# Kernel tuning notes

Measured on AMD Instinct MI355X. Metric: run time of the kernel, lower is better.

Reference implementation:

```python
import jax, jax.numpy as jnp
import numpy as np

LEAKY_SLOPE = 0.2
N_HEADS = 8
INPUT_DIM = 128
HEAD_DIM = 16  # embed_dim=128 // n_heads=8


def setup_inputs() -> dict:
    key = jax.random.key(0)
    k1, k2, k3, k4 = jax.random.split(key, 4)
    b, n = 4, 512
    h = jax.random.normal(k1, (b, n, INPUT_DIM), dtype=jnp.float32)
    mask = jnp.zeros((b, n, n), dtype=bool)  # 1 = attention not possible
    stdv_w = 1.0 / np.sqrt(HEAD_DIM)
    Wl = jax.random.uniform(k2, (N_HEADS, INPUT_DIM, HEAD_DIM), minval=-stdv_w, maxval=stdv_w, dtype=jnp.float32)
    Wr = jax.random.uniform(k3, (N_HEADS, INPUT_DIM, HEAD_DIM), minval=-stdv_w, maxval=stdv_w, dtype=jnp.float32)
    # Wak in torch is (n_heads, head_dim, 1); stdv = 1/sqrt(size(-1)) = 1
    Wak = jax.random.uniform(k4, (N_HEADS, HEAD_DIM), minval=-1.0, maxval=1.0, dtype=jnp.float32)
    return {"h": h, "mask": mask, "Wl": Wl, "Wr": Wr, "Wak": Wak}


def reference(h, mask, Wl, Wr, Wak):
    b, n, _ = h.shape
    # per-head projections: g = h @ W  -> (heads, batch, N, head_dim)
    g_l = jnp.einsum('bni,hid->hbnd', h, Wl)
    g_r = jnp.einsum('bni,hid->hbnd', h, Wr)
    # additive attention: LeakyReLU(g_l_i + g_r_j) . a  -> (heads, batch, N, N)
    e = jax.nn.leaky_relu(g_l[:, :, :, None, :] + g_r[:, :, None, :, :],
                          negative_slope=LEAKY_SLOPE)
    scores = jnp.einsum('hbijd,hd->hbij', e, Wak)
    scores = jnp.where(mask[None], -jnp.inf, scores)
    attn = jax.nn.softmax(scores, axis=-1)
    # weighted sum of g_r, then ReLU; output layout (batch, N, heads*head_dim)
    h_prime = jax.nn.relu(jnp.einsum('hbij,hbjd->bihd', attn, g_r))
    return h_prime.reshape(b, n, -1)
```

## Files before the change

### kernel.cpp

```cpp
#include <hip/hip_runtime.h>
#include <hip/hip_bf16.h>

#define B_SZ 4
#define N_SZ 512
#define IN_DIM 128
#define NH 8
#define HD 16
#define SLOPE 0.2f

#define ROWS 32
#define JT   16
#define TPB  512
#define GR_STRIDE 18
#define HROW (IN_DIM + 1)

typedef float v2f __attribute__((ext_vector_type(2)));


__global__ __launch_bounds__(256) void proj_kernel(
    const float* __restrict__ hin, const float* __restrict__ Wl,
    const float* __restrict__ Wr, float* __restrict__ gl, float* __restrict__ gr)
{
    int row = blockIdx.x;
    __shared__ float hrow[IN_DIM];
    int t = threadIdx.x;
    if (t < IN_DIM) hrow[t] = hin[(size_t)row * IN_DIM + t];
    __syncthreads();

    int side = t >> 7;
    int hd = t & 127;
    int head = hd >> 4, d = hd & 15;
    const float* W = (side ? Wr : Wl) + head * (IN_DIM * HD) + d;
    float acc = 0.f;
#pragma unroll 16
    for (int k = 0; k < IN_DIM; ++k)
        acc = fmaf(hrow[k], W[k * HD], acc);

    int b = row >> 9, i = row & (N_SZ - 1);
    float* g = side ? gr : gl;
    g[((size_t)(head * B_SZ + b) * N_SZ + i) * HD + d] = acc;
}

__global__ __launch_bounds__(TPB, 4) void attn_kernel(
    const float* __restrict__ gl, const float* __restrict__ gr,
    const float* __restrict__ Wak, const unsigned char* __restrict__ mask,
    float* __restrict__ out)
{
    __shared__ float grs[N_SZ * GR_STRIDE];
    __shared__ float gls[ROWS * HD];
    __shared__ float crs[N_SZ];

    int bid = blockIdx.x;
    int itile = bid & 15;
    int hb = bid >> 4;
    int head = hb >> 2, b = hb & 3;
    int t = threadIdx.x;

    const float* grp = gr + (size_t)hb * (N_SZ * HD);
    for (int idx4 = t; idx4 < N_SZ * HD / 4; idx4 += TPB) {
        float4 v = ((const float4*)grp)[idx4];
        int j = idx4 >> 2, dq = (idx4 & 3) * 4;
        float* p = &grs[j * GR_STRIDE + dq];
        *(v2f*)p = (v2f){v.x, v.y};
        *(v2f*)(p + 2) = (v2f){v.z, v.w};
    }
    const float* glp = gl + ((size_t)hb * N_SZ + itile * ROWS) * HD;
    gls[t] = glp[t];
    __syncthreads();

    const float* ap = Wak + head * HD;

    {
        const float* r = &grs[t * GR_STRIDE];
        float acc = 0.f;
#pragma unroll
        for (int dd = 0; dd < HD; ++dd) acc = fmaf(ap[dd], r[dd], acc);
        crs[t] = 0.6f * acc;
    }
    __syncthreads();

    int il = t >> 4;
    int jt = t & 15;
    int i = itile * ROWS + il;

    v2f glv[HD / 2], o[HD / 2];
    float av04[HD];
    const float* grow = &gls[il * HD];
#pragma unroll
    for (int e = 0; e < HD / 2; ++e) glv[e] = *(const v2f*)(grow + 2 * e);
    float cl06;
    {
        float acc = 0.f;
#pragma unroll
        for (int dd = 0; dd < HD; ++dd) acc = fmaf(ap[dd], grow[dd], acc);
        cl06 = 0.6f * acc;
    }
#pragma unroll
    for (int dd = 0; dd < HD; ++dd) av04[dd] = 0.4f * ap[dd];
#pragma unroll
    for (int e = 0; e < HD / 2; ++e) o[e] = (v2f){0.f, 0.f};

    const unsigned char* mrow = mask + ((size_t)(b * N_SZ + i)) * N_SZ;
    unsigned mbits = 0;
#pragma unroll
    for (int jj = 0; jj < N_SZ / JT; ++jj)
        mbits |= (mrow[jj * JT + jt] ? 1u : 0u) << jj;

    float l = 0.f;

#pragma unroll 4
    for (int jj = 0; jj < N_SZ / JT; ++jj) {
        int j = jj * JT + jt;
        const float* r = &grs[j * GR_STRIDE];
        v2f gj[HD / 2];
#pragma unroll
        for (int e = 0; e < HD / 2; ++e) gj[e] = *(const v2f*)(r + 2 * e);

        v2f xv[HD / 2];
#pragma unroll
        for (int e = 0; e < HD / 2; ++e) xv[e] = glv[e] + gj[e];

        float s0 = cl06 + crs[j];
        float s1 = 0.f;
#pragma unroll
        for (int e = 0; e < HD / 2; ++e) {
            s0 = fmaf(av04[2 * e],     fabsf(xv[e].x), s0);
            s1 = fmaf(av04[2 * e + 1], fabsf(xv[e].y), s1);
        }
        float s = fminf(s0 + s1, 80.f);
        if (mbits & (1u << jj)) s = -1e30f;

        float p = __expf(s);
        l += p;
        v2f pv = (v2f){p, p};
#pragma unroll
        for (int e = 0; e < HD / 2; ++e)
            o[e] += pv * gj[e];
    }

#pragma unroll
    for (int off = 1; off < JT; off <<= 1) {
        l += __shfl_xor(l, off, 64);
#pragma unroll
        for (int e = 0; e < HD / 2; ++e) {
            v2f other;
            other.x = __shfl_xor(o[e].x, off, 64);
            other.y = __shfl_xor(o[e].y, off, 64);
            o[e] += other;
        }
    }

    if (jt == 0) {
        float inv = 1.f / l;
        float res[HD];
#pragma unroll
        for (int e = 0; e < HD / 2; ++e) {
            res[2 * e]     = fmaxf(o[e].x * inv, 0.f);
            res[2 * e + 1] = fmaxf(o[e].y * inv, 0.f);
        }
        float* op = out + ((size_t)(b * N_SZ + i)) * (NH * HD) + head * HD;
        *(float4*)op = *(float4*)res;
        *(float4*)(op + 4) = *(float4*)(res + 4);
        *(float4*)(op + 8) = *(float4*)(res + 8);
        *(float4*)(op + 12) = *(float4*)(res + 12);
    }
}


__global__ __launch_bounds__(TPB) void gatv2_fused(
    const float* __restrict__ hin, const unsigned char* __restrict__ mask,
    const float* __restrict__ Wl, const float* __restrict__ Wr,
    const float* __restrict__ Wak, float* __restrict__ out)
{
    __shared__ float wrs[IN_DIM * HD];
    __shared__ float hsh[ROWS][HROW];
    __shared__ float grs[N_SZ * GR_STRIDE];
    __shared__ float gls[ROWS][HD];

    int bid = blockIdx.x;
    int itile = bid & 15;
    int hb = bid >> 4;
    int head = hb >> 2, b = hb & 3;
    int t = threadIdx.x;

    int jl = t >> 4;
    int d  = t & 15;

    for (int idx = t; idx < IN_DIM * HD; idx += TPB)
        wrs[idx] = Wr[head * IN_DIM * HD + idx];

    const float* hb_base = hin + (size_t)b * N_SZ * IN_DIM;
    const float* wlcol = Wl + head * IN_DIM * HD + d;

    for (int c = 0; c < N_SZ / ROWS; ++c) {
        __syncthreads();
        const float* hc = hb_base + (size_t)c * ROWS * IN_DIM;
        for (int idx = t; idx < ROWS * IN_DIM; idx += TPB)
            hsh[idx >> 7][idx & 127] = hc[idx];
        __syncthreads();

        float acc = 0.f;
#pragma unroll 16
        for (int k = 0; k < IN_DIM; ++k)
            acc = fmaf(hsh[jl][k], wrs[k * HD + d], acc);
        grs[(c * ROWS + jl) * GR_STRIDE + d] = acc;

        if (c == itile) {
            float accl = 0.f;
#pragma unroll 16
            for (int k = 0; k < IN_DIM; ++k)
                accl = fmaf(hsh[jl][k], wlcol[k * HD], accl);
            gls[jl][d] = accl;
        }
    }
    __syncthreads();

    int il = jl;
    int jt = d;
    int i = itile * ROWS + il;

    float glv[HD], avv[HD];
#pragma unroll
    for (int dd = 0; dd < HD; ++dd) glv[dd] = gls[il][dd];
    const float* ap = Wak + head * HD;
#pragma unroll
    for (int dd = 0; dd < HD; ++dd) avv[dd] = ap[dd];

    const unsigned char* mrow = mask + ((size_t)(b * N_SZ + i)) * N_SZ;

    float m = -1e30f, l = 0.f;
    float o[HD];
#pragma unroll
    for (int dd = 0; dd < HD; ++dd) o[dd] = 0.f;

    for (int jj = 0; jj < N_SZ / JT; ++jj) {
        int j = jj * JT + jt;
        const float* r = &grs[j * GR_STRIDE];
        float gj[HD];
#pragma unroll
        for (int e = 0; e < HD / 2; ++e) {
            float2 v = *(const float2*)(r + 2 * e);
            gj[2 * e] = v.x; gj[2 * e + 1] = v.y;
        }

        float s = 0.f;
#pragma unroll
        for (int dd = 0; dd < HD; ++dd) {
            float x = glv[dd] + gj[dd];
            float lr = fmaxf(x, SLOPE * x);
            s = fmaf(avv[dd], lr, s);
        }
        if (mrow[j]) s = -1e30f;

        float mn = fmaxf(m, s);
        float cc = __expf(m - mn);
        float p = __expf(s - mn);
        l = fmaf(l, cc, p);
#pragma unroll
        for (int dd = 0; dd < HD; ++dd)
            o[dd] = fmaf(o[dd], cc, p * gj[dd]);
        m = mn;
    }

#pragma unroll
    for (int off = 1; off < JT; off <<= 1) {
        float mo = __shfl_xor(m, off, 64);
        float lo = __shfl_xor(l, off, 64);
        float mn = fmaxf(m, mo);
        float c1 = __expf(m - mn), c2 = __expf(mo - mn);
        l = l * c1 + lo * c2;
#pragma unroll
        for (int dd = 0; dd < HD; ++dd)
            o[dd] = o[dd] * c1 + __shfl_xor(o[dd], off, 64) * c2;
        m = mn;
    }

    if (jt == 0) {
        float inv = 1.f / l;
        float res[HD];
#pragma unroll
        for (int dd = 0; dd < HD; ++dd)
            res[dd] = fmaxf(o[dd] * inv, 0.f);
        float* op = out + ((size_t)(b * N_SZ + i)) * (NH * HD) + head * HD;
#pragma unroll
        for (int e = 0; e < HD / 4; ++e)
            *(float4*)(op + 4 * e) = *(float4*)(res + 4 * e);
    }
}

extern "C" void kernel_launch(void* const* d_in, const int* in_sizes, int n_in,
                              void* d_out, int out_size, void* d_ws, size_t ws_size,
                              hipStream_t stream) {
    const float* hin = (const float*)d_in[0];
    const unsigned char* mask = (const unsigned char*)d_in[1];
    const float* Wl = (const float*)d_in[2];
    const float* Wr = (const float*)d_in[3];
    const float* Wak = (const float*)d_in[4];
    float* out = (float*)d_out;
    (void)in_sizes; (void)n_in; (void)out_size;

    const size_t g_elems = (size_t)NH * B_SZ * N_SZ * HD;
    const size_t need = 2 * g_elems * sizeof(float);

    if (ws_size >= need && d_ws != nullptr) {
        float* gl = (float*)d_ws;
        float* gr = gl + g_elems;
        proj_kernel<<<B_SZ * N_SZ, 256, 0, stream>>>(hin, Wl, Wr, gl, gr);
        attn_kernel<<<NH * B_SZ * (N_SZ / ROWS), TPB, 0, stream>>>(
            gl, gr, Wak, mask, out);
    } else {
        gatv2_fused<<<NH * B_SZ * (N_SZ / ROWS), TPB, 0, stream>>>(
            hin, mask, Wl, Wr, Wak, out);
    }
}
```

Before: 91.82 us.

## Split attention over key segments with partial sums and a combine kernel

The attention kernel now splits the 512 keys into two segments per block. The grid doubles to 1024 blocks, and each block stores its unnormalized output and sum into workspace. A new combine kernel adds the partials, normalizes and applies ReLU. The change also raises the occupancy hint to 8, pads the gr shared stride to 20 for float4 LDS loads, and folds the 0.4 scale outside the dot. The aim is more parallelism and occupancy, at the cost of an extra launch, more workspace traffic, and a larger workspace requirement that could fall back to the fused path.

Result: slower. 153.3 us (+66.9%).

```diff
diff --git a/kernel.cpp b/kernel.cpp
--- a/kernel.cpp
+++ b/kernel.cpp
@@ -10,12 +10,19 @@
 
 #define ROWS 32
 #define JT   16
+#define JSEG 2
+#define JB   (N_SZ / JSEG)
 #define TPB  512
-#define GR_STRIDE 18
+#define GR_STRIDE 20
 #define HROW (IN_DIM + 1)
 
 typedef float v2f __attribute__((ext_vector_type(2)));
 
+#define WS_GL 0
+#define WS_GR (NH * B_SZ * N_SZ * HD)
+#define WS_OP (2 * WS_GR)
+#define WS_LP (WS_OP + NH * B_SZ * JSEG * N_SZ * HD)
+#define WS_TOT (WS_LP + NH * B_SZ * JSEG * N_SZ)
 
 __global__ __launch_bounds__(256) void proj_kernel(
     const float* __restrict__ hin, const float* __restrict__ Wl,
@@ -41,23 +48,25 @@
     g[((size_t)(head * B_SZ + b) * N_SZ + i) * HD + d] = acc;
 }
 
-__global__ __launch_bounds__(TPB, 4) void attn_kernel(
+__global__ __launch_bounds__(TPB, 8) void attn_part_kernel(
     const float* __restrict__ gl, const float* __restrict__ gr,
     const float* __restrict__ Wak, const unsigned char* __restrict__ mask,
-    float* __restrict__ out)
+    float* __restrict__ opart, float* __restrict__ lpart)
 {
-    __shared__ float grs[N_SZ * GR_STRIDE];
+    __shared__ float grs[JB * GR_STRIDE];
     __shared__ float gls[ROWS * HD];
-    __shared__ float crs[N_SZ];
+    __shared__ float crs[JB];
 
     int bid = blockIdx.x;
-    int itile = bid & 15;
-    int hb = bid >> 4;
+    int seg = bid & (JSEG - 1);
+    int itile = (bid >> 1) & 15;
+    int hb = bid >> 5;
     int head = hb >> 2, b = hb & 3;
     int t = threadIdx.x;
-
-    const float* grp = gr + (size_t)hb * (N_SZ * HD);
-    for (int idx4 = t; idx4 < N_SZ * HD / 4; idx4 += TPB) {
+    int j0 = seg * JB;
+
+    const float* grp = gr + ((size_t)hb * N_SZ + j0) * HD;
+    for (int idx4 = t; idx4 < JB * HD / 4; idx4 += TPB) {
         float4 v = ((const float4*)grp)[idx4];
         int j = idx4 >> 2, dq = (idx4 & 3) * 4;
         float* p = &grs[j * GR_STRIDE + dq];
@@ -70,21 +79,19 @@
 
     const float* ap = Wak + head * HD;
 
-    {
+    if (t < JB) {
         const float* r = &grs[t * GR_STRIDE];
         float acc = 0.f;
 #pragma unroll
         for (int dd = 0; dd < HD; ++dd) acc = fmaf(ap[dd], r[dd], acc);
         crs[t] = 0.6f * acc;
     }
-    __syncthreads();
 
     int il = t >> 4;
     int jt = t & 15;
     int i = itile * ROWS + il;
 
     v2f glv[HD / 2], o[HD / 2];
-    float av04[HD];
     const float* grow = &gls[il * HD];
 #pragma unroll
     for (int e = 0; e < HD / 2; ++e) glv[e] = *(const v2f*)(grow + 2 * e);
@@ -96,38 +103,44 @@
         cl06 = 0.6f * acc;
     }
 #pragma unroll
-    for (int dd = 0; dd < HD; ++dd) av04[dd] = 0.4f * ap[dd];
-#pragma unroll
     for (int e = 0; e < HD / 2; ++e) o[e] = (v2f){0.f, 0.f};
 
-    const unsigned char* mrow = mask + ((size_t)(b * N_SZ + i)) * N_SZ;
+    const unsigned char* mrow = mask + ((size_t)(b * N_SZ + i)) * N_SZ + j0;
     unsigned mbits = 0;
 #pragma unroll
-    for (int jj = 0; jj < N_SZ / JT; ++jj)
+    for (int jj = 0; jj < JB / JT; ++jj)
         mbits |= (mrow[jj * JT + jt] ? 1u : 0u) << jj;
 
+    __syncthreads();
+
     float l = 0.f;
 
 #pragma unroll 4
-    for (int jj = 0; jj < N_SZ / JT; ++jj) {
+    for (int jj = 0; jj < JB / JT; ++jj) {
         int j = jj * JT + jt;
         const float* r = &grs[j * GR_STRIDE];
-        v2f gj[HD / 2];
-#pragma unroll
-        for (int e = 0; e < HD / 2; ++e) gj[e] = *(const v2f*)(r + 2 * e);
+        float4 g01 = *(const float4*)(r);
+        float4 g23 = *(const float4*)(r + 4);
+        float4 g45 = *(const float4*)(r + 8);
+        float4 g67 = *(const float4*)(r + 12);
+        v2f gj[HD / 2] = {
+            (v2f){g01.x, g01.y}, (v2f){g01.z, g01.w},
+            (v2f){g23.x, g23.y}, (v2f){g23.z, g23.w},
+            (v2f){g45.x, g45.y}, (v2f){g45.z, g45.w},
+            (v2f){g67.x, g67.y}, (v2f){g67.z, g67.w}};
 
         v2f xv[HD / 2];
 #pragma unroll
         for (int e = 0; e < HD / 2; ++e) xv[e] = glv[e] + gj[e];
 
-        float s0 = cl06 + crs[j];
-        float s1 = 0.f;
+        float s0 = 0.f, s1 = 0.f;
 #pragma unroll
         for (int e = 0; e < HD / 2; ++e) {
-            s0 = fmaf(av04[2 * e],     fabsf(xv[e].x), s0);
-            s1 = fmaf(av04[2 * e + 1], fabsf(xv[e].y), s1);
-        }
-        float s = fminf(s0 + s1, 80.f);
+            s0 = fmaf(ap[2 * e],     fabsf(xv[e].x), s0);
+            s1 = fmaf(ap[2 * e + 1], fabsf(xv[e].y), s1);
+        }
+        float s = fmaf(0.4f, s0 + s1, cl06 + crs[j]);
+        s = fminf(s, 80.f);
         if (mbits & (1u << jj)) s = -1e30f;
 
         float p = __expf(s);
@@ -151,21 +164,35 @@
     }
 
     if (jt == 0) {
-        float inv = 1.f / l;
         float res[HD];
 #pragma unroll
-        for (int e = 0; e < HD / 2; ++e) {
-            res[2 * e]     = fmaxf(o[e].x * inv, 0.f);
-            res[2 * e + 1] = fmaxf(o[e].y * inv, 0.f);
-        }
-        float* op = out + ((size_t)(b * N_SZ + i)) * (NH * HD) + head * HD;
+        for (int e = 0; e < HD / 2; ++e) { res[2 * e] = o[e].x; res[2 * e + 1] = o[e].y; }
+        float* op = opart + ((size_t)(hb * JSEG + seg) * N_SZ + i) * HD;
         *(float4*)op = *(float4*)res;
         *(float4*)(op + 4) = *(float4*)(res + 4);
         *(float4*)(op + 8) = *(float4*)(res + 8);
         *(float4*)(op + 12) = *(float4*)(res + 12);
-    }
-}
-
+        lpart[(size_t)(hb * JSEG + seg) * N_SZ + i] = l;
+    }
+}
+
+__global__ __launch_bounds__(256) void combine_kernel(
+    const float* __restrict__ opart, const float* __restrict__ lpart,
+    float* __restrict__ out)
+{
+    int gid = blockIdx.x * 256 + threadIdx.x;
+    int d = gid & 15;
+    int r = gid >> 4;
+    int i = r & (N_SZ - 1);
+    int hb = r >> 9;
+    int head = hb >> 2, b = hb & 3;
+
+    float o = opart[((size_t)(hb * JSEG + 0) * N_SZ + i) * HD + d]
+            + opart[((size_t)(hb * JSEG + 1) * N_SZ + i) * HD + d];
+    float l = lpart[(size_t)(hb * JSEG + 0) * N_SZ + i]
+            + lpart[(size_t)(hb * JSEG + 1) * N_SZ + i];
+    out[((size_t)(b * N_SZ + i)) * (NH * HD) + head * HD + d] = fmaxf(o / l, 0.f);
+}
 
 __global__ __launch_bounds__(TPB) void gatv2_fused(
     const float* __restrict__ hin, const unsigned char* __restrict__ mask,
@@ -174,7 +201,7 @@
 {
     __shared__ float wrs[IN_DIM * HD];
     __shared__ float hsh[ROWS][HROW];
-    __shared__ float grs[N_SZ * GR_STRIDE];
+    __shared__ float grs[N_SZ * 18];
     __shared__ float gls[ROWS][HD];
 
     int bid = blockIdx.x;
@@ -203,7 +230,7 @@
 #pragma unroll 16
         for (int k = 0; k < IN_DIM; ++k)
             acc = fmaf(hsh[jl][k], wrs[k * HD + d], acc);
-        grs[(c * ROWS + jl) * GR_STRIDE + d] = acc;
+        grs[(c * ROWS + jl) * 18 + d] = acc;
 
         if (c == itile) {
             float accl = 0.f;
@@ -235,7 +262,7 @@
 
     for (int jj = 0; jj < N_SZ / JT; ++jj) {
         int j = jj * JT + jt;
-        const float* r = &grs[j * GR_STRIDE];
+        const float* r = &grs[j * 18];
         float gj[HD];
 #pragma unroll
         for (int e = 0; e < HD / 2; ++e) {
@@ -299,15 +326,19 @@
     float* out = (float*)d_out;
     (void)in_sizes; (void)n_in; (void)out_size;
 
-    const size_t g_elems = (size_t)NH * B_SZ * N_SZ * HD;
-    const size_t need = 2 * g_elems * sizeof(float);
+    const size_t need = (size_t)WS_TOT * sizeof(float);
 
     if (ws_size >= need && d_ws != nullptr) {
-        float* gl = (float*)d_ws;
-        float* gr = gl + g_elems;
+        float* ws = (float*)d_ws;
+        float* gl = ws + WS_GL;
+        float* gr = ws + WS_GR;
+        float* op = ws + WS_OP;
+        float* lp = ws + WS_LP;
         proj_kernel<<<B_SZ * N_SZ, 256, 0, stream>>>(hin, Wl, Wr, gl, gr);
-        attn_kernel<<<NH * B_SZ * (N_SZ / ROWS), TPB, 0, stream>>>(
-            gl, gr, Wak, mask, out);
+        attn_part_kernel<<<NH * B_SZ * 16 * JSEG, TPB, 0, stream>>>(
+            gl, gr, Wak, mask, op, lp);
+        combine_kernel<<<(NH * B_SZ * N_SZ * HD) / 256, 256, 0, stream>>>(
+            op, lp, out);
     } else {
         gatv2_fused<<<NH * B_SZ * (N_SZ / ROWS), TPB, 0, stream>>>(
             hin, mask, Wl, Wr, Wak, out);
```
